# Kernel optimization log

Hardware: AMD Instinct MI355X
Metric: run time of the kernel (lower is better)

## Reference

```python
import jax, jax.numpy as jnp
import numpy as np

NSAMPLE = 32  # knn neighbors (init kwarg nsample)
BN_EPS = 1e-5


def _mlp_layer(x, w, b, g, beta, m, v):
    # x: [B,S,K,Cin]; 1x1 conv == channel matmul, then eval-mode BN, then ReLU
    h = jnp.einsum('bskc,oc->bsko', x, w) + b
    h = (h - m) * (g * jax.lax.rsqrt(v + BN_EPS)) + beta
    return jax.nn.relu(h)


def setup_inputs() -> dict:
    key = jax.random.key(0)
    ks = jax.random.split(key, 8)
    B, N, D, S = 8, 16384, 64, 2048
    inp = {
        'xyz': jax.random.normal(ks[0], (B, N, 3), jnp.float32),
        'points': jax.random.normal(ks[1], (B, N, D), jnp.float32),
        'sample_idx': jax.random.randint(ks[2], (S,), 0, N, jnp.int32),
        'w0': jax.random.normal(ks[3], (64, 64), jnp.float32) * 0.1,
        'b0': jnp.zeros((64,), jnp.float32),
        'g0': jnp.ones((64,), jnp.float32),
        'beta0': jnp.zeros((64,), jnp.float32),
        'm0': jnp.zeros((64,), jnp.float32),
        'v0': jnp.ones((64,), jnp.float32),
        'w1': jax.random.normal(ks[4], (64, 64), jnp.float32) * 0.1,
        'b1': jnp.zeros((64,), jnp.float32),
        'g1': jnp.ones((64,), jnp.float32),
        'beta1': jnp.zeros((64,), jnp.float32),
        'm1': jnp.zeros((64,), jnp.float32),
        'v1': jnp.ones((64,), jnp.float32),
        'w2': jax.random.normal(ks[5], (128, 64), jnp.float32) * 0.1,
        'b2': jnp.zeros((128,), jnp.float32),
        'g2': jnp.ones((128,), jnp.float32),
        'beta2': jnp.zeros((128,), jnp.float32),
        'm2': jnp.zeros((128,), jnp.float32),
        'v2': jnp.ones((128,), jnp.float32),
    }
    return inp


def reference(xyz, points, sample_idx,
              w0, b0, g0, beta0, m0, v0,
              w1, b1, g1, beta1, m1, v1,
              w2, b2, g2, beta2, m2, v2):
    # subsample (torch.randperm analogue, shared across batch)
    new_xyz = xyz[:, sample_idx, :]            # [B,S,3]
    new_pts = points[:, sample_idx, :]         # [B,S,D]
    # squared distances in feature space: [B,S,N]
    d = (jnp.sum(new_pts * new_pts, -1)[:, :, None]
         - 2.0 * jnp.einsum('bsd,bnd->bsn', new_pts, points)
         + jnp.sum(points * points, -1)[:, None, :])
    _, idx = jax.lax.top_k(-d, NSAMPLE)        # k smallest -> [B,S,K]
    # gather neighbors: [B,S,K,D]
    grouped = jax.vmap(lambda p, i: p[i])(points, idx)
    h = _mlp_layer(grouped, w0, b0, g0, beta0, m0, v0)
    h = _mlp_layer(h, w1, b1, g1, beta1, m1, v1)
    h = _mlp_layer(h, w2, b2, g2, beta2, m2, v2)
    new_points = jnp.max(h, axis=2)            # max over neighbors -> [B,S,128]
    return (new_xyz, new_points)
```

## Files before the change

### kernel.cpp

```cpp
#include <hip/hip_runtime.h>

#define B_  8
#define N_  16384
#define D_  64
#define S_  2048
#define K_  32
#define SPLIT_  4
#define NSPL_   (N_/SPLIT_)
#define CH32_   (NSPL_/32)
#define PLANE_  ((size_t)B_*N_*64)

using short8_ = __attribute__((ext_vector_type(8))) short;
using short4_ = __attribute__((ext_vector_type(4))) short;
using f32x4_  = __attribute__((ext_vector_type(4))) float;

__device__ __forceinline__ void bf3split(float f, short& h0, short& h1, short& h2)
{
  unsigned u0 = __float_as_uint(f);
  float f0 = __uint_as_float(u0 & 0xFFFF0000u);
  h0 = (short)(u0 >> 16);
  float r1 = f - f0;
  unsigned u1 = __float_as_uint(r1);
  float f1 = __uint_as_float(u1 & 0xFFFF0000u);
  h1 = (short)(u1 >> 16);
  float r2 = r1 - f1;
  h2 = (short)(__float_as_uint(r2) >> 16);
}

__device__ __forceinline__ void bf2split1(float f, short& h0, short& h1)
{
  unsigned u = __float_as_uint(f);
  h0 = (short)(u >> 16);
  float r = f - __uint_as_float(u & 0xFFFF0000u);
  h1 = (short)(__float_as_uint(r) >> 16);
}

__device__ __forceinline__ void bf2split8(const float* f, short8_& h0, short8_& h1)
{
  #pragma unroll
  for (int j = 0; j < 8; ++j) {
    unsigned u = __float_as_uint(f[j]);
    h0[j] = (short)(u >> 16);
    float r = f[j] - __uint_as_float(u & 0xFFFF0000u);
    h1[j] = (short)(__float_as_uint(r) >> 16);
  }
}

__device__ __forceinline__ void insert32(float (&Lv)[32], int (&Li)[32], float x, int n)
{
  bool ci = x < Lv[0];
  #pragma unroll
  for (int i = 0; i < 31; ++i) {
    bool c1 = x < Lv[i+1];
    float nv = c1 ? Lv[i+1] : (ci ? x : Lv[i]);
    int   ni = c1 ? Li[i+1] : (ci ? n : Li[i]);
    Lv[i] = nv; Li[i] = ni;
    ci = c1;
  }
  Lv[31] = ci ? x : Lv[31];
  Li[31] = ci ? n : Li[31];
}

__global__ __launch_bounds__(256) void k_prep(
    const float* __restrict__ xyz, const float* __restrict__ points,
    const int* __restrict__ sidx, float* __restrict__ out, float* __restrict__ sqn,
    short* __restrict__ P0, short* __restrict__ P1, short* __restrict__ P2,
    const float* __restrict__ w0, const float* __restrict__ b0,
    const float* __restrict__ g0, const float* __restrict__ be0,
    const float* __restrict__ m0, const float* __restrict__ v0,
    const float* __restrict__ w1, const float* __restrict__ b1,
    const float* __restrict__ g1, const float* __restrict__ be1,
    const float* __restrict__ m1, const float* __restrict__ v1,
    const float* __restrict__ w2, const float* __restrict__ b2,
    const float* __restrict__ g2, const float* __restrict__ be2,
    const float* __restrict__ m2, const float* __restrict__ v2,
    short* __restrict__ Ws0_0, short* __restrict__ Ws0_1,
    short* __restrict__ Ws1_0, short* __restrict__ Ws1_1,
    short* __restrict__ Ws2_0, short* __restrict__ Ws2_1,
    float* __restrict__ bia0, float* __restrict__ bia1, float* __restrict__ bia2)
{
  int tid = blockIdx.x * 256 + threadIdx.x;
  const float4* p = (const float4*)(points + (size_t)tid * 64);

  float s = 0.f;
  #pragma unroll
  for (int i = 0; i < 16; ++i) {
    float4 v = p[i];
    s += v.x*v.x + v.y*v.y + v.z*v.z + v.w*v.w;
  }
  sqn[tid] = s;

  int n = tid & (N_-1);
  int c = n >> 6, ct = (n >> 4) & 3, mc = n & 15;
  size_t segbase = (((size_t)(tid >> 14) * 256 + c) * 4 + ct) * 2;

  #pragma unroll
  for (int g = 0; g < 8; ++g) {
    float4 a = p[2*g], b4 = p[2*g+1];
    float f[8] = {a.x,a.y,a.z,a.w, b4.x,b4.y,b4.z,b4.w};
    short8_ h0v, h1v, h2v;
    #pragma unroll
    for (int j = 0; j < 8; ++j) {
      short h0, h1, h2;
      bf3split(f[j], h0, h1, h2);
      h0v[j] = h0; h1v[j] = h1; h2v[j] = h2;
    }
    size_t off = ((segbase + (g>>2))*64 + (size_t)(g&3)*16 + mc)*8;
    *(short8_*)(P0 + off) = h0v;
    *(short8_*)(P1 + off) = h1v;
    *(short8_*)(P2 + off) = h2v;
  }
  if (tid < B_*S_) {
    int b = tid >> 11, ss = tid & (S_-1);
    int nn = sidx[ss];
    const float* src = xyz + ((size_t)b * N_ + nn) * 3;
    out[(size_t)tid*3+0] = src[0];
    out[(size_t)tid*3+1] = src[1];
    out[(size_t)tid*3+2] = src[2];
  }
  if (tid < 16384) {
    float wval, sc; short *d0, *d1; int i = tid;
    if (tid < 4096) {
      int o = tid >> 6;
      sc = g0[o] * rsqrtf(v0[o] + 1e-5f);
      wval = w0[tid]; d0 = Ws0_0; d1 = Ws0_1;
    } else if (tid < 8192) {
      i = tid - 4096; int o = i >> 6;
      sc = g1[o] * rsqrtf(v1[o] + 1e-5f);
      wval = w1[i]; d0 = Ws1_0; d1 = Ws1_1;
    } else {
      i = tid - 8192; int o = i >> 6;
      sc = g2[o] * rsqrtf(v2[o] + 1e-5f);
      wval = w2[i]; d0 = Ws2_0; d1 = Ws2_1;
    }
    short h0, h1;
    bf2split1(wval * sc, h0, h1);
    d0[i] = h0; d1[i] = h1;
  }
  if (tid < 256) {
    if (tid < 64) {
      float sc = g0[tid] * rsqrtf(v0[tid] + 1e-5f);
      bia0[tid] = (b0[tid] - m0[tid]) * sc + be0[tid];
    } else if (tid < 128) {
      int j = tid - 64;
      float sc = g1[j] * rsqrtf(v1[j] + 1e-5f);
      bia1[j] = (b1[j] - m1[j]) * sc + be1[j];
    } else {
      int j = tid - 128;
      float sc = g2[j] * rsqrtf(v2[j] + 1e-5f);
      bia2[j] = (b2[j] - m2[j]) * sc + be2[j];
    }
  }
}

__global__ __launch_bounds__(256) void k_knn(
    const short* __restrict__ P0, const short* __restrict__ P1,
    const short* __restrict__ P2, const int* __restrict__ sidx,
    const float* __restrict__ sqn, uint2* __restrict__ pw)
{
  __shared__ __align__(16) char smraw[33280];
  float* Dtr = (float*)smraw;
  uint2* qb  = (uint2*)(smraw + 9216);

  const int t = threadIdx.x;
  const int b     = blockIdx.x & 7;
  const int y     = blockIdx.x >> 3;
  const int tile  = y & 31;
  const int split = y >> 5;
  const int s0 = tile * 64;
  const float* Qb = sqn + (size_t)b * N_;

  const int lane = t & 63, wv = t >> 6;
  const int quad = lane >> 4, mcol = lane & 15;

  short8_ A0[2], A1[2], A2[2];
  {
    int srow = sidx[s0 + 16*wv + mcol];
    int cs = srow >> 6, cts = (srow >> 4) & 3, ms = srow & 15;
    size_t ab = (((size_t)(b*256 + cs))*4 + cts)*2*512 + ((size_t)quad*16 + ms)*8;
    #pragma unroll
    for (int kt = 0; kt < 2; ++kt) {
      A0[kt] = *(const short8_*)(P0 + ab + kt*512);
      A1[kt] = *(const short8_*)(P1 + ab + kt*512);
      A2[kt] = *(const short8_*)(P2 + ab + kt*512);
    }
  }

  float Lv[32]; int Li[32];
  #pragma unroll
  for (int i = 0; i < 32; ++i) { Lv[i] = 3.0e38f; Li[i] = 0; }

  const int r = t >> 2;
  const int q = t & 3;
  const int n0base = split * NSPL_;
  const size_t bc8base = (size_t)b * 256;

  int qhead = 0, qtail = 0;

  auto do_select = [&](int n0sel) {
    float ownL0 = Lv[0];
    float t24 = Lv[24];
    t24 = fmaxf(t24, __shfl_xor(t24, 1));
    t24 = fmaxf(t24, __shfl_xor(t24, 2));
    const float thr = fminf(t24, ownL0);

    float4 ka = *(const float4*)(Dtr + r*36 + q*8);
    float4 kb = *(const float4*)(Dtr + r*36 + q*8 + 4);
    float x8[8] = {ka.x,ka.y,ka.z,ka.w, kb.x,kb.y,kb.z,kb.w};
    unsigned m = 0;
    #pragma unroll
    for (int i = 0; i < 8; ++i)
      m |= (x8[i] < thr) ? (1u << i) : 0u;
    while (m) {
      int i = __ffs(m) - 1;
      m &= m - 1;
      float xlo = (i & 1) ? ((i & 2) ? x8[3] : x8[1]) : ((i & 2) ? x8[2] : x8[0]);
      float xhi = (i & 1) ? ((i & 2) ? x8[7] : x8[5]) : ((i & 2) ? x8[6] : x8[4]);
      float x = (i & 4) ? xhi : xlo;
      if (qtail - qhead >= 8) {
        uint2 e = qb[(qhead & 7)*256 + t];
        qhead++;
        float xe = __uint_as_float(e.x);
        if (xe < Lv[0])
          insert32(Lv, Li, xe, (int)e.y);
      }
      qb[(qtail & 7)*256 + t] = make_uint2(__float_as_uint(x), (unsigned)(n0sel + q*8 + i));
      qtail++;
    }
    if (__any((qtail - qhead) >= 2)) {
      if (qhead < qtail) {
        uint2 e = qb[(qhead & 7)*256 + t];
        qhead++;
        float x = __uint_as_float(e.x);
        if (x < Lv[0])
          insert32(Lv, Li, x, (int)e.y);
      }
    }
  };

  size_t goff = ((bc8base + (size_t)(n0base >> 6)) * 8) * 512 + (size_t)lane * 8;

  short8_ b0[2][2], b1[2][2], b2[2][2];
  float sq0, sq1;

  auto kload = [&](int n0c) {
    #pragma unroll
    for (int s = 0; s < 4; ++s) {
      b0[s>>1][s&1] = *(const short8_*)(P0 + goff + (size_t)s*512);
      b1[s>>1][s&1] = *(const short8_*)(P1 + goff + (size_t)s*512);
      b2[s>>1][s&1] = *(const short8_*)(P2 + goff + (size_t)s*512);
    }
    sq0 = Qb[n0c + mcol];
    sq1 = Qb[n0c + 16 + mcol];
    goff += 2048;
  };

  auto kmfma = [&]() {
    #pragma unroll
    for (int ct = 0; ct < 2; ++ct) {
      f32x4_ a = {0.f, 0.f, 0.f, 0.f};
      #pragma unroll
      for (int kt = 0; kt < 2; ++kt) {
        a = __builtin_amdgcn_mfma_f32_16x16x32_bf16(A0[kt], b0[ct][kt], a, 0,0,0);
        a = __builtin_amdgcn_mfma_f32_16x16x32_bf16(A0[kt], b1[ct][kt], a, 0,0,0);
        a = __builtin_amdgcn_mfma_f32_16x16x32_bf16(A1[kt], b0[ct][kt], a, 0,0,0);
        a = __builtin_amdgcn_mfma_f32_16x16x32_bf16(A1[kt], b1[ct][kt], a, 0,0,0);
        a = __builtin_amdgcn_mfma_f32_16x16x32_bf16(A0[kt], b2[ct][kt], a, 0,0,0);
        a = __builtin_amdgcn_mfma_f32_16x16x32_bf16(A2[kt], b0[ct][kt], a, 0,0,0);
        a = __builtin_amdgcn_mfma_f32_16x16x32_bf16(A1[kt], b2[ct][kt], a, 0,0,0);
        a = __builtin_amdgcn_mfma_f32_16x16x32_bf16(A2[kt], b1[ct][kt], a, 0,0,0);
      }
      int cc = 16*ct + mcol;
      float sq = ct ? sq1 : sq0;
      int rb = 16*wv + 4*quad;
      Dtr[(rb+0)*36 + cc] = sq - 2.f*a[0];
      Dtr[(rb+1)*36 + cc] = sq - 2.f*a[1];
      Dtr[(rb+2)*36 + cc] = sq - 2.f*a[2];
      Dtr[(rb+3)*36 + cc] = sq - 2.f*a[3];
    }
  };

  #define FILLJ(J) { \
    float4 ka = *(const float4*)(Dtr + r*36 + q*8); \
    float4 kb = *(const float4*)(Dtr + r*36 + q*8 + 4); \
    float x8f[8] = {ka.x,ka.y,ka.z,ka.w, kb.x,kb.y,kb.z,kb.w}; \
    _Pragma("unroll") \
    for (int i = 0; i < 8; ++i) { \
      Lv[(J)*8 + i] = x8f[i]; \
      Li[(J)*8 + i] = n0base + (J)*32 + q*8 + i; } }

  kload(n0base + 0*32);            kmfma();
  kload(n0base + 1*32); FILLJ(0);  kmfma();
  kload(n0base + 2*32); FILLJ(1);  kmfma();
  kload(n0base + 3*32); FILLJ(2);  kmfma();
  kload(n0base + 4*32); FILLJ(3);
  #pragma unroll
  for (int k = 2; k <= 32; k <<= 1) {
    #pragma unroll
    for (int j2 = k >> 1; j2 > 0; j2 >>= 1) {
      #pragma unroll
      for (int i = 0; i < 32; ++i) {
        int l = i ^ j2;
        if (l > i) {
          bool g = (Lv[l] > Lv[i]) || (Lv[l] == Lv[i] && Li[l] > Li[i]);
          bool sw = ((i & k) == 0) ? g : !g;
          float tv = sw ? Lv[l] : Lv[i];
          float uv = sw ? Lv[i] : Lv[l];
          int   ti = sw ? Li[l] : Li[i];
          int   ui = sw ? Li[i] : Li[l];
          Lv[i] = tv; Lv[l] = uv; Li[i] = ti; Li[l] = ui;
        }
      }
    }
  }
  kmfma();

  for (int ch = 5; ch < CH32_; ++ch) {
    kload(n0base + ch*32);
    do_select(n0base + ch*32 - 32);
    kmfma();
  }
  do_select(n0base + NSPL_ - 32);

  while (__any(qhead < qtail)) {
    if (qhead < qtail) {
      uint2 e = qb[(qhead & 7)*256 + t];
      qhead++;
      float x = __uint_as_float(e.x);
      if (x < Lv[0])
        insert32(Lv, Li, x, (int)e.y);
    }
  }

  uint2* mbuf = (uint2*)smraw;
  const int rowg = b * S_ + s0;
  for (int pass = 0; pass < 2; ++pass) {
    __syncthreads();
    const int rb = pass * 32;
    if (r >= rb && r < rb + 32) {
      #pragma unroll
      for (int i = 0; i < 32; ++i)
        mbuf[(r - rb)*130 + q*32 + (31 - i)] =
            make_uint2(__float_as_uint(Lv[i]), (unsigned)Li[i]);
    }
    __syncthreads();
    if (t < 32) {
      const uint2* Lrow = mbuf + t*130;
      uint2* dst = pw + ((size_t)(rowg + rb + t) * SPLIT_ + split) * 32;
      int p0 = 0, p1 = 0, p2 = 0, p3 = 0;
      for (int k = 0; k < 32; ++k) {
        float bv = 3.0e38f; unsigned bi = 0xFFFFFFFFu; int bq = 0;
        int pa[4] = {p0, p1, p2, p3};
        #pragma unroll
        for (int q4 = 0; q4 < 4; ++q4) {
          if (pa[q4] < 32) {
            uint2 e = Lrow[q4*32 + pa[q4]];
            float v = __uint_as_float(e.x);
            if (v < bv || (v == bv && e.y < bi)) { bv = v; bi = e.y; bq = q4; }
          }
        }
        dst[k] = make_uint2(__float_as_uint(bv), bi);
        if (bq == 0) p0++; else if (bq == 1) p1++; else if (bq == 2) p2++; else p3++;
      }
    }
  }
  #undef FILLJ
}

__global__ __launch_bounds__(256) void k_prep_fb(
    const float* __restrict__ xyz, const float* __restrict__ points,
    const int* __restrict__ sidx, float* __restrict__ out, float* __restrict__ sqn)
{
  int tid = blockIdx.x * 256 + threadIdx.x;
  const float4* p = (const float4*)(points + (size_t)tid * 64);
  float s = 0.f;
  #pragma unroll
  for (int i = 0; i < 16; ++i) {
    float4 v = p[i];
    s += v.x*v.x + v.y*v.y + v.z*v.z + v.w*v.w;
  }
  sqn[tid] = s;
  if (tid < B_*S_) {
    int b = tid >> 11, ss = tid & (S_-1);
    int n = sidx[ss];
    const float* src = xyz + ((size_t)b * N_ + n) * 3;
    out[(size_t)tid*3+0] = src[0];
    out[(size_t)tid*3+1] = src[1];
    out[(size_t)tid*3+2] = src[2];
  }
}

__global__ __launch_bounds__(256) void k_knn_fb(
    const float* __restrict__ points, const int* __restrict__ sidx,
    const float* __restrict__ sqn, uint2* __restrict__ pw)
{
  __shared__ __align__(16) char smraw[45312];
  short* Bp0 = (short*)smraw;
  short* Bp1 = (short*)(smraw + 9216);
  short* Bp2 = (short*)(smraw + 18432);
  float* Dt  = (float*)(smraw + 27648);
  float* sqc = (float*)(smraw + 45056);

  const int t = threadIdx.x;
  const int b     = blockIdx.x & 7;
  const int y     = blockIdx.x >> 3;
  const int tile  = y & 31;
  const int split = y >> 5;
  const int s0 = tile * 64;
  const float* Pb = points + (size_t)b * N_ * 64;
  const float* Qb = sqn    + (size_t)b * N_;

  const int lane = t & 63, wv = t >> 6;
  const int quad = lane >> 4, mcol = lane & 15;

  short8_ A0[2], A1[2], A2[2];
  {
    int srow = sidx[s0 + 16*wv + mcol];
    const float* ar = Pb + (size_t)srow * 64;
    #pragma unroll
    for (int kt = 0; kt < 2; ++kt) {
      float4 v0 = *(const float4*)(ar + 32*kt + 8*quad);
      float4 v1 = *(const float4*)(ar + 32*kt + 8*quad + 4);
      float f[8] = {v0.x,v0.y,v0.z,v0.w,v1.x,v1.y,v1.z,v1.w};
      #pragma unroll
      for (int j = 0; j < 8; ++j) {
        short h0, h1, h2;
        bf3split(f[j], h0, h1, h2);
        A0[kt][j] = h0; A1[kt][j] = h1; A2[kt][j] = h2;
      }
    }
  }

  float Lv[32]; int Li[32];
  #pragma unroll
  for (int i = 0; i < 32; ++i) { Lv[i] = 3.0e38f; Li[i] = 0; }

  const int r = t >> 2;
  const int q = t & 3;
  const int n0base = split * NSPL_;

  for (int ch = 0; ch < NSPL_/64; ++ch) {
    const int n0 = n0base + ch * 64;
    {
      const int n = t & 63, jg = t >> 6;
      const float* src = Pb + (size_t)(n0 + n) * 64 + 16*jg;
      float4 u0 = *(const float4*)(src);
      float4 u1 = *(const float4*)(src + 4);
      float4 u2 = *(const float4*)(src + 8);
      float4 u3 = *(const float4*)(src + 12);
      float f[16] = {u0.x,u0.y,u0.z,u0.w, u1.x,u1.y,u1.z,u1.w,
                     u2.x,u2.y,u2.z,u2.w, u3.x,u3.y,u3.z,u3.w};
      short8_ p0[2], p1[2], p2[2];
      #pragma unroll
      for (int j = 0; j < 16; ++j) {
        short h0, h1, h2;
        bf3split(f[j], h0, h1, h2);
        p0[j>>3][j&7] = h0; p1[j>>3][j&7] = h1; p2[j>>3][j&7] = h2;
      }
      *(short8_*)(Bp0 + n*72 + 16*jg)     = p0[0];
      *(short8_*)(Bp0 + n*72 + 16*jg + 8) = p0[1];
      *(short8_*)(Bp1 + n*72 + 16*jg)     = p1[0];
      *(short8_*)(Bp1 + n*72 + 16*jg + 8) = p1[1];
      *(short8_*)(Bp2 + n*72 + 16*jg)     = p2[0];
      *(short8_*)(Bp2 + n*72 + 16*jg + 8) = p2[1];
      if (t < 16) *(float4*)(sqc + 4*t) = *(const float4*)(Qb + n0 + 4*t);
    }
    __syncthreads();

    f32x4_ acc[4];
    #pragma unroll
    for (int ct = 0; ct < 4; ++ct) {
      const int boff = (16*ct + mcol)*72 + 8*quad;
      short8_ b0[2], b1[2], b2[2];
      b0[0] = *(const short8_*)(Bp0 + boff); b0[1] = *(const short8_*)(Bp0 + boff + 32);
      b1[0] = *(const short8_*)(Bp1 + boff); b1[1] = *(const short8_*)(Bp1 + boff + 32);
      b2[0] = *(const short8_*)(Bp2 + boff); b2[1] = *(const short8_*)(Bp2 + boff + 32);
      f32x4_ a = {0.f, 0.f, 0.f, 0.f};
      #pragma unroll
      for (int kt = 0; kt < 2; ++kt) {
        a = __builtin_amdgcn_mfma_f32_16x16x32_bf16(A0[kt], b0[kt], a, 0,0,0);
        a = __builtin_amdgcn_mfma_f32_16x16x32_bf16(A0[kt], b1[kt], a, 0,0,0);
        a = __builtin_amdgcn_mfma_f32_16x16x32_bf16(A1[kt], b0[kt], a, 0,0,0);
        a = __builtin_amdgcn_mfma_f32_16x16x32_bf16(A1[kt], b1[kt], a, 0,0,0);
        a = __builtin_amdgcn_mfma_f32_16x16x32_bf16(A0[kt], b2[kt], a, 0,0,0);
        a = __builtin_amdgcn_mfma_f32_16x16x32_bf16(A2[kt], b0[kt], a, 0,0,0);
        a = __builtin_amdgcn_mfma_f32_16x16x32_bf16(A1[kt], b2[kt], a, 0,0,0);
        a = __builtin_amdgcn_mfma_f32_16x16x32_bf16(A2[kt], b1[kt], a, 0,0,0);
      }
      acc[ct] = a;
    }
    #pragma unroll
    for (int ct = 0; ct < 4; ++ct) {
      int c = 16*ct + mcol;
      float sq = sqc[c];
      float4 kv;
      kv.x = sq - 2.f*acc[ct][0];
      kv.y = sq - 2.f*acc[ct][1];
      kv.z = sq - 2.f*acc[ct][2];
      kv.w = sq - 2.f*acc[ct][3];
      *(float4*)(Dt + c*68 + 16*wv + 4*quad) = kv;
    }
    __syncthreads();

    float L0 = Lv[0];
    L0 = fminf(L0, __shfl_xor(L0, 1));
    L0 = fminf(L0, __shfl_xor(L0, 2));
    const float tau = L0;
    #pragma unroll
    for (int g = 0; g < 4; ++g) {
      #pragma unroll
      for (int u = 0; u < 4; ++u) {
        int c = q*16 + g*4 + u;
        float x = Dt[c*68 + r];
        if (x < fminf(tau, Lv[0]))
          insert32(Lv, Li, x, n0 + c);
      }
    }
  }

  uint2* mbuf = (uint2*)smraw;
  const int rowg = b * S_ + s0;
  for (int pass = 0; pass < 2; ++pass) {
    __syncthreads();
    const int rb = pass * 32;
    if (r >= rb && r < rb + 32) {
      #pragma unroll
      for (int i = 0; i < 32; ++i)
        mbuf[(r - rb)*130 + q*32 + (31 - i)] =
            make_uint2(__float_as_uint(Lv[i]), (unsigned)Li[i]);
    }
    __syncthreads();
    if (t < 32) {
      const uint2* Lrow = mbuf + t*130;
      uint2* dst = pw + ((size_t)(rowg + rb + t) * SPLIT_ + split) * 32;
      int p0 = 0, p1 = 0, p2 = 0, p3 = 0;
      for (int k = 0; k < 32; ++k) {
        float bv = 3.0e38f; unsigned bi = 0xFFFFFFFFu; int bq = 0;
        int pa[4] = {p0, p1, p2, p3};
        #pragma unroll
        for (int q4 = 0; q4 < 4; ++q4) {
          if (pa[q4] < 32) {
            uint2 e = Lrow[q4*32 + pa[q4]];
            float v = __uint_as_float(e.x);
            if (v < bv || (v == bv && e.y < bi)) { bv = v; bi = e.y; bq = q4; }
          }
        }
        dst[k] = make_uint2(__float_as_uint(bv), bi);
        if (bq == 0) p0++; else if (bq == 1) p1++; else if (bq == 2) p2++; else p3++;
      }
    }
  }
}

__device__ __forceinline__ void layer_pre(
    int lane, int wv, const short* Xa0, const short* Xa1,
    short* Ha0, short* Ha1,
    const short* __restrict__ Ws0, const short* __restrict__ Ws1,
    const float* __restrict__ biaP)
{
  const int quad = lane >> 4, mcol = lane & 15;
  const int o = wv*16 + mcol;
  short8_ B0[2], B1[2];
  #pragma unroll
  for (int kt = 0; kt < 2; ++kt) {
    B0[kt] = *(const short8_*)(Ws0 + o*64 + kt*32 + quad*8);
    B1[kt] = *(const short8_*)(Ws1 + o*64 + kt*32 + quad*8);
  }
  const float bo = biaP[o];
  const int kt2 = (o >> 5) & 1, qk2 = (o >> 3) & 3, h2 = (o >> 2) & 1, j2 = o & 3;
  #pragma unroll
  for (int mt = 0; mt < 2; ++mt) {
    short8_ A0[2], A1[2];
    #pragma unroll
    for (int kt = 0; kt < 2; ++kt) {
      A0[kt] = *(const short8_*)(Xa0 + ((mt*2+kt)*64 + lane)*8);
      A1[kt] = *(const short8_*)(Xa1 + ((mt*2+kt)*64 + lane)*8);
    }
    f32x4_ a = {0.f, 0.f, 0.f, 0.f};
    #pragma unroll
    for (int kt = 0; kt < 2; ++kt) {
      a = __builtin_amdgcn_mfma_f32_16x16x32_bf16(A0[kt], B0[kt], a, 0,0,0);
      a = __builtin_amdgcn_mfma_f32_16x16x32_bf16(A0[kt], B1[kt], a, 0,0,0);
      a = __builtin_amdgcn_mfma_f32_16x16x32_bf16(A1[kt], B0[kt], a, 0,0,0);
    }
    #pragma unroll
    for (int reg = 0; reg < 4; ++reg) {
      int ml = quad*4 + reg;
      float hval = fmaxf(a[reg] + bo, 0.f);
      short h0, h1;
      bf2split1(hval, h0, h1);
      int idx = ((mt*2 + kt2)*64 + qk2*16 + ml)*8 + h2*4 + j2;
      Ha0[idx] = h0;
      Ha1[idx] = h1;
    }
  }
}

__global__ __launch_bounds__(256) void k_mlp(
    const float* __restrict__ points, const uint2* __restrict__ pw,
    const short* __restrict__ Ws0_0, const short* __restrict__ Ws0_1,
    const short* __restrict__ Ws1_0, const short* __restrict__ Ws1_1,
    const short* __restrict__ Ws2_0, const short* __restrict__ Ws2_1,
    const float* __restrict__ bia0, const float* __restrict__ bia1,
    const float* __restrict__ bia2, float* __restrict__ out)
{
  __shared__ __align__(16) short Xa0[2048];
  __shared__ __align__(16) short Xa1[2048];
  __shared__ __align__(16) short Ha0[2048];
  __shared__ __align__(16) short Ha1[2048];
  __shared__ int   nIx[32];
  __shared__ __align__(8) uint2 Lr[128];

  const int t  = threadIdx.x;
  const int bs = blockIdx.x;
  const int b  = bs >> 11;
  const int lane = t & 63, wv = t >> 6;
  const int quad = lane >> 4, mcol = lane & 15;

  if (t < 128) Lr[t] = pw[(size_t)bs * (SPLIT_*32) + t];
  __syncthreads();
  if (t < 128) {
    uint2 e = Lr[t];
    float ev = __uint_as_float(e.x);
    int rank = t & 31;
    #pragma unroll
    for (int oq = 1; oq < 4; ++oq) {
      const uint2* L = Lr + ((((t >> 5) + oq) & 3) << 5);
      int lo = 0;
      #pragma unroll
      for (int stp = 16; stp > 0; stp >>= 1) {
        uint2 c = L[lo + stp - 1];
        float cv = __uint_as_float(c.x);
        bool lt = (cv < ev) || (cv == ev && c.y < e.y);
        lo += lt ? stp : 0;
      }
      {
        uint2 c = L[lo];
        float cv = __uint_as_float(c.x);
        bool lt = (cv < ev) || (cv == ev && c.y < e.y);
        lo += lt ? 1 : 0;
      }
      rank += lo;
    }
    if (rank < 32) nIx[rank] = (int)e.y;
  }
  __syncthreads();
  #pragma unroll
  for (int rep = 0; rep < 2; ++rep) {
    int task = rep*256 + t;
    int row = task >> 4, j4 = task & 15;
    float4 v = *(const float4*)(points + ((size_t)b*N_ + nIx[row])*64 + j4*4);
    int kt = j4 >> 3, qk = (j4 >> 1) & 3, h = j4 & 1;
    int base = (((row>>4)*2 + kt)*64 + qk*16 + (row&15))*8 + h*4;
    float f4[4] = {v.x, v.y, v.z, v.w};
    short4_ s0v, s1v;
    #pragma unroll
    for (int e = 0; e < 4; ++e) {
      short h0, h1;
      bf2split1(f4[e], h0, h1);
      s0v[e] = h0; s1v[e] = h1;
    }
    *(short4_*)(Xa0 + base) = s0v;
    *(short4_*)(Xa1 + base) = s1v;
  }
  __syncthreads();

  layer_pre(lane, wv, Xa0, Xa1, Ha0, Ha1, Ws0_0, Ws0_1, bia0);
  __syncthreads();
  layer_pre(lane, wv, Ha0, Ha1, Xa0, Xa1, Ws1_0, Ws1_1, bia1);
  __syncthreads();

  short8_ A0[2][2], A1[2][2];
  #pragma unroll
  for (int mt = 0; mt < 2; ++mt)
    #pragma unroll
    for (int kt = 0; kt < 2; ++kt) {
      A0[mt][kt] = *(const short8_*)(Xa0 + ((mt*2+kt)*64 + lane)*8);
      A1[mt][kt] = *(const short8_*)(Xa1 + ((mt*2+kt)*64 + lane)*8);
    }
  float* outp = out + (size_t)(B_*S_)*3 + (size_t)bs*128;
  #pragma unroll
  for (int sub = 0; sub < 2; ++sub) {
    const int o = (wv*2 + sub)*16 + mcol;
    short8_ B0[2], B1[2];
    #pragma unroll
    for (int kt = 0; kt < 2; ++kt) {
      B0[kt] = *(const short8_*)(Ws2_0 + o*64 + kt*32 + quad*8);
      B1[kt] = *(const short8_*)(Ws2_1 + o*64 + kt*32 + quad*8);
    }
    float vmax = -3.0e38f;
    #pragma unroll
    for (int mt = 0; mt < 2; ++mt) {
      f32x4_ a = {0.f, 0.f, 0.f, 0.f};
      #pragma unroll
      for (int kt = 0; kt < 2; ++kt) {
        a = __builtin_amdgcn_mfma_f32_16x16x32_bf16(A0[mt][kt], B0[kt], a, 0,0,0);
        a = __builtin_amdgcn_mfma_f32_16x16x32_bf16(A0[mt][kt], B1[kt], a, 0,0,0);
        a = __builtin_amdgcn_mfma_f32_16x16x32_bf16(A1[mt][kt], B0[kt], a, 0,0,0);
      }
      vmax = fmaxf(vmax, fmaxf(fmaxf(a[0], a[1]), fmaxf(a[2], a[3])));
    }
    vmax = fmaxf(vmax, __shfl_xor(vmax, 16));
    vmax = fmaxf(vmax, __shfl_xor(vmax, 32));
    if (quad == 0) outp[o] = fmaxf(vmax + bia2[o], 0.f);
  }
}

__device__ __forceinline__ void layer_mfma(
    int lane, int wv, const float* Xf, float* Hf,
    const float* __restrict__ wgt, const float* scl, const float* bia)
{
  const int quad = lane >> 4, mcol = lane & 15;
  const int o = wv*16 + mcol;
  const float sc = scl[o];
  short8_ B0[2], B1[2];
  #pragma unroll
  for (int kt = 0; kt < 2; ++kt) {
    const float* wp = wgt + o*64 + kt*32 + quad*8;
    float4 u0 = *(const float4*)(wp);
    float4 u1 = *(const float4*)(wp + 4);
    float f[8] = {u0.x*sc,u0.y*sc,u0.z*sc,u0.w*sc,
                  u1.x*sc,u1.y*sc,u1.z*sc,u1.w*sc};
    bf2split8(f, B0[kt], B1[kt]);
  }
  const float bo = bia[o];
  const int kt2 = (o >> 5) & 1, qk2 = (o >> 3) & 3, h2 = (o >> 2) & 1, j2 = o & 3;
  #pragma unroll
  for (int mt = 0; mt < 2; ++mt) {
    short8_ A0[2], A1[2];
    #pragma unroll
    for (int kt = 0; kt < 2; ++kt) {
      float4 x0 = *(const float4*)(Xf + (((mt*2+kt)*2+0)*256) + lane*4);
      float4 x1 = *(const float4*)(Xf + (((mt*2+kt)*2+1)*256) + lane*4);
      float f[8] = {x0.x,x0.y,x0.z,x0.w, x1.x,x1.y,x1.z,x1.w};
      bf2split8(f, A0[kt], A1[kt]);
    }
    f32x4_ a = {0.f, 0.f, 0.f, 0.f};
    #pragma unroll
    for (int kt = 0; kt < 2; ++kt) {
      a = __builtin_amdgcn_mfma_f32_16x16x32_bf16(A0[kt], B0[kt], a, 0,0,0);
      a = __builtin_amdgcn_mfma_f32_16x16x32_bf16(A0[kt], B1[kt], a, 0,0,0);
      a = __builtin_amdgcn_mfma_f32_16x16x32_bf16(A1[kt], B0[kt], a, 0,0,0);
    }
    #pragma unroll
    for (int reg = 0; reg < 4; ++reg) {
      int ml = quad*4 + reg;
      float hval = fmaxf(a[reg] + bo, 0.f);
      Hf[((mt*2 + kt2)*2 + h2)*256 + (qk2*16 + ml)*4 + j2] = hval;
    }
  }
}

__global__ __launch_bounds__(256) void k_mlp_fb(
    const float* __restrict__ points, const uint2* __restrict__ pw,
    const float* __restrict__ w0, const float* __restrict__ b0,
    const float* __restrict__ g0, const float* __restrict__ be0,
    const float* __restrict__ m0, const float* __restrict__ v0,
    const float* __restrict__ w1, const float* __restrict__ b1,
    const float* __restrict__ g1, const float* __restrict__ be1,
    const float* __restrict__ m1, const float* __restrict__ v1,
    const float* __restrict__ w2, const float* __restrict__ b2,
    const float* __restrict__ g2, const float* __restrict__ be2,
    const float* __restrict__ m2, const float* __restrict__ v2,
    float* __restrict__ out)
{
  __shared__ __align__(16) float Xf[2048];
  __shared__ __align__(16) float Hf[2048];
  __shared__ float scl[128];
  __shared__ float bia[128];
  __shared__ int   nIx[32];
  __shared__ __align__(8) uint2 Lr[128];

  const int t  = threadIdx.x;
  const int bs = blockIdx.x;
  const int b  = bs >> 11;
  const int lane = t & 63, wv = t >> 6;
  const int quad = lane >> 4, mcol = lane & 15;

  if (t < 128) Lr[t] = pw[(size_t)bs * (SPLIT_*32) + t];
  if (t >= 128) {
    int i = t - 128;
    float sc = g0[i] * rsqrtf(v0[i] + 1e-5f);
    scl[i] = sc;
    bia[i] = (b0[i] - m0[i]) * sc + be0[i];
  }
  __syncthreads();
  if (t < 128) {
    uint2 e = Lr[t];
    float ev = __uint_as_float(e.x);
    int rank = t & 31;
    #pragma unroll
    for (int oq = 1; oq < 4; ++oq) {
      const uint2* L = Lr + ((((t >> 5) + oq) & 3) << 5);
      int lo = 0;
      #pragma unroll
      for (int stp = 16; stp > 0; stp >>= 1) {
        uint2 c = L[lo + stp - 1];
        float cv = __uint_as_float(c.x);
        bool lt = (cv < ev) || (cv == ev && c.y < e.y);
        lo += lt ? stp : 0;
      }
      {
        uint2 c = L[lo];
        float cv = __uint_as_float(c.x);
        bool lt = (cv < ev) || (cv == ev && c.y < e.y);
        lo += lt ? 1 : 0;
      }
      rank += lo;
    }
    if (rank < 32) nIx[rank] = (int)e.y;
  }
  __syncthreads();
  #pragma unroll
  for (int rep = 0; rep < 2; ++rep) {
    int task = rep*256 + t;
    int row = task >> 4, j4 = task & 15;
    float4 v = *(const float4*)(points + ((size_t)b*N_ + nIx[row])*64 + j4*4);
    int kt = j4 >> 3, qk = (j4 >> 1) & 3, h = j4 & 1;
    *(float4*)(Xf + (((row>>4)*2 + kt)*2 + h)*256 + (qk*16 + (row&15))*4) = v;
  }
  __syncthreads();

  layer_mfma(lane, wv, Xf, Hf, w0, scl, bia);
  __syncthreads();
  if (t < 64) {
    float sc = g1[t] * rsqrtf(v1[t] + 1e-5f);
    scl[t] = sc;
    bia[t] = (b1[t] - m1[t]) * sc + be1[t];
  }
  __syncthreads();
  layer_mfma(lane, wv, Hf, Xf, w1, scl, bia);
  __syncthreads();
  if (t < 128) {
    float sc = g2[t] * rsqrtf(v2[t] + 1e-5f);
    scl[t] = sc;
    bia[t] = (b2[t] - m2[t]) * sc + be2[t];
  }
  __syncthreads();

  short8_ A0[2][2], A1[2][2];
  #pragma unroll
  for (int mt = 0; mt < 2; ++mt)
    #pragma unroll
    for (int kt = 0; kt < 2; ++kt) {
      float4 x0 = *(const float4*)(Xf + (((mt*2+kt)*2+0)*256) + lane*4);
      float4 x1 = *(const float4*)(Xf + (((mt*2+kt)*2+1)*256) + lane*4);
      float f[8] = {x0.x,x0.y,x0.z,x0.w, x1.x,x1.y,x1.z,x1.w};
      bf2split8(f, A0[mt][kt], A1[mt][kt]);
    }
  float* outp = out + (size_t)(B_*S_)*3 + (size_t)bs*128;
  #pragma unroll
  for (int sub = 0; sub < 2; ++sub) {
    const int o = (wv*2 + sub)*16 + mcol;
    const float sc = scl[o];
    short8_ B0[2], B1[2];
    #pragma unroll
    for (int kt = 0; kt < 2; ++kt) {
      const float* wp = w2 + o*64 + kt*32 + quad*8;
      float4 u0 = *(const float4*)(wp);
      float4 u1 = *(const float4*)(wp + 4);
      float f[8] = {u0.x*sc,u0.y*sc,u0.z*sc,u0.w*sc,
                    u1.x*sc,u1.y*sc,u1.z*sc,u1.w*sc};
      bf2split8(f, B0[kt], B1[kt]);
    }
    float vmax = -3.0e38f;
    #pragma unroll
    for (int mt = 0; mt < 2; ++mt) {
      f32x4_ a = {0.f, 0.f, 0.f, 0.f};
      #pragma unroll
      for (int kt = 0; kt < 2; ++kt) {
        a = __builtin_amdgcn_mfma_f32_16x16x32_bf16(A0[mt][kt], B0[kt], a, 0,0,0);
        a = __builtin_amdgcn_mfma_f32_16x16x32_bf16(A0[mt][kt], B1[kt], a, 0,0,0);
        a = __builtin_amdgcn_mfma_f32_16x16x32_bf16(A1[mt][kt], B0[kt], a, 0,0,0);
      }
      vmax = fmaxf(vmax, fmaxf(fmaxf(a[0], a[1]), fmaxf(a[2], a[3])));
    }
    vmax = fmaxf(vmax, __shfl_xor(vmax, 16));
    vmax = fmaxf(vmax, __shfl_xor(vmax, 32));
    if (quad == 0) outp[o] = fmaxf(vmax + bia[o], 0.f);
  }
}

extern "C" void kernel_launch(void* const* d_in, const int* in_sizes, int n_in,
                              void* d_out, int out_size, void* d_ws, size_t ws_size,
                              hipStream_t stream)
{
  const float* xyz  = (const float*)d_in[0];
  const float* pts  = (const float*)d_in[1];
  const int*   sidx = (const int*)  d_in[2];
  const float* w0 = (const float*)d_in[3];
  const float* b0 = (const float*)d_in[4];
  const float* g0 = (const float*)d_in[5];
  const float* be0= (const float*)d_in[6];
  const float* m0 = (const float*)d_in[7];
  const float* v0 = (const float*)d_in[8];
  const float* w1 = (const float*)d_in[9];
  const float* b1 = (const float*)d_in[10];
  const float* g1 = (const float*)d_in[11];
  const float* be1= (const float*)d_in[12];
  const float* m1 = (const float*)d_in[13];
  const float* v1 = (const float*)d_in[14];
  const float* w2 = (const float*)d_in[15];
  const float* b2 = (const float*)d_in[16];
  const float* g2 = (const float*)d_in[17];
  const float* be2= (const float*)d_in[18];
  const float* m2 = (const float*)d_in[19];
  const float* v2 = (const float*)d_in[20];

  float* out = (float*)d_out;
  float* sqn = (float*)d_ws;
  char*  nb  = (char*)d_ws + (size_t)B_*N_*4;
  short* Ws0_0 = (short*)nb;
  short* Ws0_1 = Ws0_0 + 4096;
  short* Ws1_0 = Ws0_1 + 4096;
  short* Ws1_1 = Ws1_0 + 4096;
  short* Ws2_0 = Ws1_1 + 4096;
  short* Ws2_1 = Ws2_0 + 8192;
  float* bia0  = (float*)(Ws2_1 + 8192);
  float* bia1  = bia0 + 64;
  float* bia2  = bia1 + 64;
  uint2* pw  = (uint2*)((char*)d_ws + (size_t)B_*N_*4 + (size_t)B_*S_*K_*4);
  char*  pl  = (char*)d_ws + (size_t)B_*N_*4 + (size_t)B_*S_*K_*4
             + (size_t)B_*S_*SPLIT_*32*8;
  short* P0 = (short*)pl;
  short* P1 = P0 + PLANE_;
  short* P2 = P1 + PLANE_;
  const size_t need = (size_t)B_*N_*4 + (size_t)B_*S_*K_*4
                    + (size_t)B_*S_*SPLIT_*32*8 + 3*PLANE_*2;

  if (ws_size >= need) {
    k_prep<<<(B_*N_)/256, 256, 0, stream>>>(xyz, pts, sidx, out, sqn, P0, P1, P2,
              w0,b0,g0,be0,m0,v0, w1,b1,g1,be1,m1,v1, w2,b2,g2,be2,m2,v2,
              Ws0_0,Ws0_1, Ws1_0,Ws1_1, Ws2_0,Ws2_1, bia0,bia1,bia2);
    k_knn <<<B_*32*SPLIT_, 256, 0, stream>>>(P0, P1, P2, sidx, sqn, pw);
    k_mlp <<<B_*S_, 256, 0, stream>>>(pts, pw,
              Ws0_0,Ws0_1, Ws1_0,Ws1_1, Ws2_0,Ws2_1, bia0,bia1,bia2, out);
  } else {
    k_prep_fb<<<(B_*N_)/256, 256, 0, stream>>>(xyz, pts, sidx, out, sqn);
    k_knn_fb <<<B_*32*SPLIT_, 256, 0, stream>>>(pts, sidx, sqn, pw);
    k_mlp_fb <<<B_*S_, 256, 0, stream>>>(pts, pw,
              w0,b0,g0,be0,m0,v0, w1,b1,g1,be1,m1,v1, w2,b2,g2,be2,m2,v2, out);
  }
}
```

Before: 747.5 us.

## Swap MFMA operand order so distance tiles stay in registers, dropping LDS transpose

```diff
diff --git a/kernel.cpp b/kernel.cpp
--- a/kernel.cpp
+++ b/kernel.cpp
@@ -153,14 +153,13 @@
   }
 }
 
-__global__ __launch_bounds__(256) void k_knn(
+__global__ __launch_bounds__(256, 4) void k_knn(
     const short* __restrict__ P0, const short* __restrict__ P1,
     const short* __restrict__ P2, const int* __restrict__ sidx,
     const float* __restrict__ sqn, uint2* __restrict__ pw)
 {
   __shared__ __align__(16) char smraw[33280];
-  float* Dtr = (float*)smraw;
-  uint2* qb  = (uint2*)(smraw + 9216);
+  uint2* qb  = (uint2*)smraw;
 
   const int t = threadIdx.x;
   const int b     = blockIdx.x & 7;
@@ -190,23 +189,20 @@
   #pragma unroll
   for (int i = 0; i < 32; ++i) { Lv[i] = 3.0e38f; Li[i] = 0; }
 
-  const int r = t >> 2;
-  const int q = t & 3;
+  const int row = 16*wv + mcol;
   const int n0base = split * NSPL_;
   const size_t bc8base = (size_t)b * 256;
 
   int qhead = 0, qtail = 0;
+  float x8[8];
 
   auto do_select = [&](int n0sel) {
     float ownL0 = Lv[0];
     float t24 = Lv[24];
-    t24 = fmaxf(t24, __shfl_xor(t24, 1));
-    t24 = fmaxf(t24, __shfl_xor(t24, 2));
+    t24 = fmaxf(t24, __shfl_xor(t24, 16));
+    t24 = fmaxf(t24, __shfl_xor(t24, 32));
     const float thr = fminf(t24, ownL0);
 
-    float4 ka = *(const float4*)(Dtr + r*36 + q*8);
-    float4 kb = *(const float4*)(Dtr + r*36 + q*8 + 4);
-    float x8[8] = {ka.x,ka.y,ka.z,ka.w, kb.x,kb.y,kb.z,kb.w};
     unsigned m = 0;
     #pragma unroll
     for (int i = 0; i < 8; ++i)
@@ -224,7 +220,8 @@
         if (xe < Lv[0])
           insert32(Lv, Li, xe, (int)e.y);
       }
-      qb[(qtail & 7)*256 + t] = make_uint2(__float_as_uint(x), (unsigned)(n0sel + q*8 + i));
+      unsigned ci = (unsigned)(n0sel + ((i >> 2) << 4) + quad*4 + (i & 3));
+      qb[(qtail & 7)*256 + t] = make_uint2(__float_as_uint(x), ci);
       qtail++;
     }
     if (__any((qtail - qhead) >= 2)) {
@@ -241,59 +238,53 @@
   size_t goff = ((bc8base + (size_t)(n0base >> 6)) * 8) * 512 + (size_t)lane * 8;
 
   short8_ b0[2][2], b1[2][2], b2[2][2];
-  float sq0, sq1;
-
-  auto kload = [&](int n0c) {
+
+  auto kload = [&]() {
     #pragma unroll
     for (int s = 0; s < 4; ++s) {
       b0[s>>1][s&1] = *(const short8_*)(P0 + goff + (size_t)s*512);
       b1[s>>1][s&1] = *(const short8_*)(P1 + goff + (size_t)s*512);
       b2[s>>1][s&1] = *(const short8_*)(P2 + goff + (size_t)s*512);
     }
-    sq0 = Qb[n0c + mcol];
-    sq1 = Qb[n0c + 16 + mcol];
     goff += 2048;
   };
 
-  auto kmfma = [&]() {
+  auto kmfma = [&](int n0c) {
+    float4 sqA = *(const float4*)(Qb + n0c + quad*4);
+    float4 sqB = *(const float4*)(Qb + n0c + 16 + quad*4);
     #pragma unroll
     for (int ct = 0; ct < 2; ++ct) {
       f32x4_ a = {0.f, 0.f, 0.f, 0.f};
       #pragma unroll
       for (int kt = 0; kt < 2; ++kt) {
-        a = __builtin_amdgcn_mfma_f32_16x16x32_bf16(A0[kt], b0[ct][kt], a, 0,0,0);
-        a = __builtin_amdgcn_mfma_f32_16x16x32_bf16(A0[kt], b1[ct][kt], a, 0,0,0);
-        a = __builtin_amdgcn_mfma_f32_16x16x32_bf16(A1[kt], b0[ct][kt], a, 0,0,0);
-        a = __builtin_amdgcn_mfma_f32_16x16x32_bf16(A1[kt], b1[ct][kt], a, 0,0,0);
-        a = __builtin_amdgcn_mfma_f32_16x16x32_bf16(A0[kt], b2[ct][kt], a, 0,0,0);
-        a = __builtin_amdgcn_mfma_f32_16x16x32_bf16(A2[kt], b0[ct][kt], a, 0,0,0);
-        a = __builtin_amdgcn_mfma_f32_16x16x32_bf16(A1[kt], b2[ct][kt], a, 0,0,0);
-        a = __builtin_amdgcn_mfma_f32_16x16x32_bf16(A2[kt], b1[ct][kt], a, 0,0,0);
-      }
-      int cc = 16*ct + mcol;
-      float sq = ct ? sq1 : sq0;
-      int rb = 16*wv + 4*quad;
-      Dtr[(rb+0)*36 + cc] = sq - 2.f*a[0];
-      Dtr[(rb+1)*36 + cc] = sq - 2.f*a[1];
-      Dtr[(rb+2)*36 + cc] = sq - 2.f*a[2];
-      Dtr[(rb+3)*36 + cc] = sq - 2.f*a[3];
+        a = __builtin_amdgcn_mfma_f32_16x16x32_bf16(b0[ct][kt], A0[kt], a, 0,0,0);
+        a = __builtin_amdgcn_mfma_f32_16x16x32_bf16(b1[ct][kt], A0[kt], a, 0,0,0);
+        a = __builtin_amdgcn_mfma_f32_16x16x32_bf16(b0[ct][kt], A1[kt], a, 0,0,0);
+        a = __builtin_amdgcn_mfma_f32_16x16x32_bf16(b1[ct][kt], A1[kt], a, 0,0,0);
+        a = __builtin_amdgcn_mfma_f32_16x16x32_bf16(b2[ct][kt], A0[kt], a, 0,0,0);
+        a = __builtin_amdgcn_mfma_f32_16x16x32_bf16(b0[ct][kt], A2[kt], a, 0,0,0);
+        a = __builtin_amdgcn_mfma_f32_16x16x32_bf16(b2[ct][kt], A1[kt], a, 0,0,0);
+        a = __builtin_amdgcn_mfma_f32_16x16x32_bf16(b1[ct][kt], A2[kt], a, 0,0,0);
+      }
+      float4 sq = ct ? sqB : sqA;
+      x8[ct*4+0] = sq.x - 2.f*a[0];
+      x8[ct*4+1] = sq.y - 2.f*a[1];
+      x8[ct*4+2] = sq.z - 2.f*a[2];
+      x8[ct*4+3] = sq.w - 2.f*a[3];
     }
   };
 
   #define FILLJ(J) { \
-    float4 ka = *(const float4*)(Dtr + r*36 + q*8); \
-    float4 kb = *(const float4*)(Dtr + r*36 + q*8 + 4); \
-    float x8f[8] = {ka.x,ka.y,ka.z,ka.w, kb.x,kb.y,kb.z,kb.w}; \
     _Pragma("unroll") \
     for (int i = 0; i < 8; ++i) { \
-      Lv[(J)*8 + i] = x8f[i]; \
-      Li[(J)*8 + i] = n0base + (J)*32 + q*8 + i; } }
-
-  kload(n0base + 0*32);            kmfma();
-  kload(n0base + 1*32); FILLJ(0);  kmfma();
-  kload(n0base + 2*32); FILLJ(1);  kmfma();
-  kload(n0base + 3*32); FILLJ(2);  kmfma();
-  kload(n0base + 4*32); FILLJ(3);
+      Lv[(J)*8 + i] = x8[i]; \
+      Li[(J)*8 + i] = n0base + (J)*32 + ((i >> 2) << 4) + quad*4 + (i & 3); } }
+
+  kload();            kmfma(n0base + 0*32);
+  kload(); FILLJ(0);  kmfma(n0base + 1*32);
+  kload(); FILLJ(1);  kmfma(n0base + 2*32);
+  kload(); FILLJ(2);  kmfma(n0base + 3*32);
+  kload(); FILLJ(3);
   #pragma unroll
   for (int k = 2; k <= 32; k <<= 1) {
     #pragma unroll
@@ -313,12 +304,12 @@
       }
     }
   }
-  kmfma();
+  kmfma(n0base + 4*32);
 
   for (int ch = 5; ch < CH32_; ++ch) {
-    kload(n0base + ch*32);
+    kload();
     do_select(n0base + ch*32 - 32);
-    kmfma();
+    kmfma(n0base + ch*32);
   }
   do_select(n0base + NSPL_ - 32);
 
@@ -337,10 +328,10 @@
   for (int pass = 0; pass < 2; ++pass) {
     __syncthreads();
     const int rb = pass * 32;
-    if (r >= rb && r < rb + 32) {
+    if (row >= rb && row < rb + 32) {
       #pragma unroll
       for (int i = 0; i < 32; ++i)
-        mbuf[(r - rb)*130 + q*32 + (31 - i)] =
+        mbuf[(row - rb)*130 + quad*32 + (31 - i)] =
             make_uint2(__float_as_uint(Lv[i]), (unsigned)Li[i]);
     }
     __syncthreads();
```

Result: slower. 1.607 ms (+115.0%).
